# Kernel optimization log

Hardware: AMD Instinct MI355X
Metric: run time of the kernel (lower is better)

Reference implementation:

```python
import jax, jax.numpy as jnp
import numpy as np

B = 262144
L, NO, NW = 5, 5, 3          # num_layers, num_ops, num_widths
AD = L * NO * NW             # arch_dim = 75
D, H = 64, 4                 # embed_dim, num_heads
HD = D // H                  # head_dim = 16
EPS = 1e-5


def _ln(x, g, b):
    m = x.mean(-1, keepdims=True)
    v = ((x - m) ** 2).mean(-1, keepdims=True)
    return (x - m) / jnp.sqrt(v + EPS) * g + b


def setup_inputs() -> dict:
    key = jax.random.key(0)
    ks = jax.random.split(key, 16)
    s = 0.05
    return {
        "hw_idx": jax.random.randint(ks[0], (B,), 0, 4),
        "op_indices": jax.random.randint(ks[1], (B, L), 0, NO),
        "width_indices": jax.random.randint(ks[2], (B, L), 0, NW),
        "hw_embed": jax.random.normal(ks[3], (4, D)) * s,
        "W1": jax.random.normal(ks[4], (128, AD)) * s, "b1": jnp.zeros((128,)),
        "W2": jax.random.normal(ks[5], (D, 128)) * s, "b2": jnp.zeros((D,)),
        "ln1_g": jnp.ones((D,)), "ln1_b": jnp.zeros((D,)),
        "in_proj_w": jax.random.normal(ks[6], (3 * D, D)) * s,
        "in_proj_b": jnp.zeros((3 * D,)),
        "out_proj_w": jax.random.normal(ks[7], (D, D)) * s,
        "out_proj_b": jnp.zeros((D,)),
        "ln2_g": jnp.ones((D,)), "ln2_b": jnp.zeros((D,)),
        "W3": jax.random.normal(ks[8], (32, D)) * s, "b3": jnp.zeros((32,)),
        "W4": jax.random.normal(ks[9], (1, 32)) * s, "b4": jnp.zeros((1,)),
    }


def reference(hw_idx, op_indices, width_indices, hw_embed, W1, b1, W2, b2,
              ln1_g, ln1_b, in_proj_w, in_proj_b, out_proj_w, out_proj_b,
              ln2_g, ln2_b, W3, b3, W4, b4):
    # hardware embedding lookup -> [B, D]
    hw_emb = hw_embed[hw_idx]
    # vectorized one-hot arch encoding: [B, L*NO*NW]
    cell = op_indices * NW + width_indices                  # [B, L]
    onehot = jax.nn.one_hot(cell, NO * NW, dtype=jnp.float32).reshape(-1, AD)
    # arch encoder MLP + LayerNorm (dropout = identity at eval)
    h = jax.nn.relu(onehot @ W1.T + b1)
    arch_emb = _ln(h @ W2.T + b2, ln1_g, ln1_b)             # [B, D]
    # combined sequence of 2 tokens: [B, 2, D]
    combined = jnp.stack([hw_emb, arch_emb], axis=1)
    # multi-head self-attention (torch MultiheadAttention, batch_first)
    qkv = combined @ in_proj_w.T + in_proj_b                # [B, 2, 3D]
    q, k, v = jnp.split(qkv, 3, axis=-1)
    q = q.reshape(-1, 2, H, HD); k = k.reshape(-1, 2, H, HD); v = v.reshape(-1, 2, H, HD)
    scores = jnp.einsum('bqhd,bkhd->bhqk', q, k) / np.sqrt(HD)
    attn = jax.nn.softmax(scores, axis=-1)
    ctx = jnp.einsum('bhqk,bkhd->bqhd', attn, v).reshape(-1, 2, D)
    attn_out = ctx @ out_proj_w.T + out_proj_b
    # residual + LayerNorm, mean-pool over the 2 tokens
    x = _ln(attn_out + combined, ln2_g, ln2_b)
    pooled = x.mean(axis=1)                                 # [B, D]
    # prediction head
    latency = jax.nn.relu(pooled @ W3.T + b3) @ W4.T + b4   # [B, 1]
    return latency
```

## Files before the change

kernel.cpp:

```cpp
#include <hip/hip_runtime.h>


using s8v = __attribute__((ext_vector_type(8))) short;
using h8  = __attribute__((ext_vector_type(8))) _Float16;
using f4  = __attribute__((ext_vector_type(4))) float;

#define WF_W1   0
#define WF_W2   12288
#define WF_IP   20480
#define WF_OP   32768
#define WF_W3   36864
#define WF_HWE  38912

#define PWS     2304

__device__ __forceinline__ unsigned short f2h(float f) {
  _Float16 h = (_Float16)f;
  return __builtin_bit_cast(unsigned short, h);
}

__device__ __forceinline__ void swz(const float* __restrict__ W,
                                    const float* __restrict__ bias,
                                    unsigned short* __restrict__ dst,
                                    int Kreal, int KS, int NT, int t, int stride) {
  const int total = KS * NT * 512;
  for (int i = t; i < total; i += stride) {
    const int j = i & 7, ln = (i >> 3) & 63, fr = i >> 9;
    const int nt = fr % NT, ks = fr / NT;
    const int n = nt * 16 + (ln & 15);
    const int k = ks * 32 + (ln >> 4) * 8 + j;
    float v = 0.f;
    if (k < Kreal) v = W[n * Kreal + k];
    else if (bias && k == Kreal) v = bias[n];
    dst[i] = f2h(v);
  }
}

__global__ void k_pre(const float* __restrict__ hwe,
                      const float* __restrict__ W1, const float* __restrict__ b1,
                      const float* __restrict__ W2,
                      const float* __restrict__ ipw, const float* __restrict__ opw,
                      const float* __restrict__ W3,
                      unsigned short* __restrict__ ws) {
  const int t = blockIdx.x * 256 + threadIdx.x;
  const int stride = gridDim.x * 256;
  swz(W1,  b1,      ws + WF_W1, 75, 3, 8, t, stride);
  swz(W2,  nullptr, ws + WF_W2, 128, 4, 4, t, stride);
  swz(ipw, nullptr, ws + WF_IP, 64, 2, 12, t, stride);
  swz(opw, nullptr, ws + WF_OP, 64, 2, 4, t, stride);
  swz(W3,  nullptr, ws + WF_W3, 64, 2, 2, t, stride);
  for (int i = t; i < 256; i += stride) ws[WF_HWE + i] = f2h(hwe[i]);
}

__global__ __launch_bounds__(256, 4) void k_fused(
    const int* __restrict__ g_hw,
    const int* __restrict__ g_op, const int* __restrict__ g_wd,
    const float* __restrict__ g_hwe,
    const float* __restrict__ g_b2,
    const float* __restrict__ g_ln1g, const float* __restrict__ g_ln1b,
    const float* __restrict__ g_ipb, const float* __restrict__ g_opb,
    const float* __restrict__ g_ln2g, const float* __restrict__ g_ln2b,
    const float* __restrict__ g_b3,  const float* __restrict__ g_W4,
    const float* __restrict__ g_b4,
    const unsigned short* __restrict__ wsf,
    float* __restrict__ g_out) {
  __shared__ __align__(16) unsigned short sm[4 * PWS];
  const int tid = threadIdx.x;
  const int wave = tid >> 6, lane = tid & 63;
  const int quad = lane >> 4, l15 = lane & 15;
  unsigned short* pw = sm + wave * PWS;
  const int m0 = (blockIdx.x * 4 + wave) * 16;

  int hwv = 0, c0 = 0, c1 = 0, c2 = 0, c3 = 0, c4 = 0;
  if (lane < 16) {
    const int smp = m0 + lane;
    hwv = g_hw[smp];
    c0 =      g_op[smp * 5 + 0] * 3 + g_wd[smp * 5 + 0];
    c1 = 15 + g_op[smp * 5 + 1] * 3 + g_wd[smp * 5 + 1];
    c2 = 30 + g_op[smp * 5 + 2] * 3 + g_wd[smp * 5 + 2];
    c3 = 45 + g_op[smp * 5 + 3] * 3 + g_wd[smp * 5 + 3];
    c4 = 60 + g_op[smp * 5 + 4] * 3 + g_wd[smp * 5 + 4];
  }
  const int t0 = __shfl(c0, l15), t1 = __shfl(c1, l15), t2 = __shfl(c2, l15);
  const int t3 = __shfl(c3, l15), t4 = __shfl(c4, l15);
  const int hwrow = __shfl(hwv, l15);

  float b2v[4], l1gv[4], l1bv[4], opbv[4], l2gv[4], l2bv[4];
#pragma unroll
  for (int nt = 0; nt < 4; ++nt) {
    const int col = nt * 16 + l15;
    b2v[nt] = g_b2[col];  l1gv[nt] = g_ln1g[col]; l1bv[nt] = g_ln1b[col];
    opbv[nt] = g_opb[col]; l2gv[nt] = g_ln2g[col]; l2bv[nt] = g_ln2b[col];
  }
  float ipbq[4], ipbvv[4];
#pragma unroll
  for (int h = 0; h < 4; ++h) {
    ipbq[h]  = g_ipb[h * 16 + l15];
    ipbvv[h] = g_ipb[(h + 8) * 16 + l15];
  }
  float b3v[2], w4vv[2];
#pragma unroll
  for (int nt = 0; nt < 2; ++nt) {
    b3v[nt] = g_b3[nt * 16 + l15];
    w4vv[nt] = g_W4[nt * 16 + l15];
  }
  const float b4v = g_b4[0];

  h8 aoh[3];
#pragma unroll
  for (int ks = 0; ks < 3; ++ks) {
    s8v a;
#pragma unroll
    for (int j = 0; j < 8; ++j) {
      const int k = ks * 32 + quad * 8 + j;
      const bool hit = (k == 75) || (k == t0) || (k == t1) || (k == t2) ||
                       (k == t3) || (k == t4);
      a[j] = hit ? (short)0x3C00 : (short)0;
    }
    aoh[ks] = __builtin_bit_cast(h8, a);
  }

#pragma unroll
  for (int nt = 0; nt < 8; ++nt) {
    f4 acc = {0.f, 0.f, 0.f, 0.f};
#pragma unroll
    for (int ks = 0; ks < 3; ++ks) {
      const h8 bf = *(const h8*)(wsf + WF_W1 + ((ks * 8 + nt) * 64 + lane) * 8);
      acc = __builtin_amdgcn_mfma_f32_16x16x32_f16(aoh[ks], bf, acc, 0, 0, 0);
    }
    const int col = nt * 16 + l15;
#pragma unroll
    for (int r = 0; r < 4; ++r) {
      float v = acc[r];
      v = v > 0.f ? v : 0.f;
      pw[(quad * 4 + r) * 136 + col] = f2h(v);
    }
  }

  h8 a2[4];
#pragma unroll
  for (int ks = 0; ks < 4; ++ks)
    a2[ks] = *(const h8*)(pw + l15 * 136 + ks * 32 + quad * 8);
  float archres[4][4];
  {
    float val[4][4];
#pragma unroll
    for (int nt = 0; nt < 4; ++nt) {
      f4 acc = {0.f, 0.f, 0.f, 0.f};
#pragma unroll
      for (int ks = 0; ks < 4; ++ks) {
        const h8 bf = *(const h8*)(wsf + WF_W2 + ((ks * 4 + nt) * 64 + lane) * 8);
        acc = __builtin_amdgcn_mfma_f32_16x16x32_f16(a2[ks], bf, acc, 0, 0, 0);
      }
#pragma unroll
      for (int r = 0; r < 4; ++r) val[nt][r] = acc[r] + b2v[nt];
    }
#pragma unroll
    for (int r = 0; r < 4; ++r) {
      float s = val[0][r] + val[1][r] + val[2][r] + val[3][r];
      float q = val[0][r] * val[0][r] + val[1][r] * val[1][r] +
                val[2][r] * val[2][r] + val[3][r] * val[3][r];
#pragma unroll
      for (int off = 1; off <= 8; off <<= 1) {
        s += __shfl_xor(s, off);
        q += __shfl_xor(q, off);
      }
      const float mean = s * (1.f / 64.f);
      const float var  = q * (1.f / 64.f) - mean * mean;
      const float rstd = rsqrtf(var + 1e-5f);
#pragma unroll
      for (int nt = 0; nt < 4; ++nt) {
        const int col = nt * 16 + l15;
        const float xn = (val[nt][r] - mean) * rstd * l1gv[nt] + l1bv[nt];
        archres[nt][r] = xn;
        pw[(quad * 4 + r) * 72 + col] = f2h(xn);
      }
    }
  }

  h8 at0[2], at1[2];
#pragma unroll
  for (int ks = 0; ks < 2; ++ks) {
    at0[ks] = *(const h8*)(wsf + WF_HWE + hwrow * 64 + ks * 32 + quad * 8);
    at1[ks] = *(const h8*)(pw + l15 * 72 + ks * 32 + quad * 8);
  }
#pragma unroll
  for (int h = 0; h < 4; ++h) {
    f4 aq0 = {0.f,0.f,0.f,0.f}, aq1 = {0.f,0.f,0.f,0.f};
    f4 ak0 = {0.f,0.f,0.f,0.f}, ak1 = {0.f,0.f,0.f,0.f};
    f4 av0 = {0.f,0.f,0.f,0.f}, av1 = {0.f,0.f,0.f,0.f};
#pragma unroll
    for (int ks = 0; ks < 2; ++ks) {
      const h8 bq = *(const h8*)(wsf + WF_IP + ((ks * 12 + h    ) * 64 + lane) * 8);
      const h8 bk = *(const h8*)(wsf + WF_IP + ((ks * 12 + h + 4) * 64 + lane) * 8);
      const h8 bv = *(const h8*)(wsf + WF_IP + ((ks * 12 + h + 8) * 64 + lane) * 8);
      aq0 = __builtin_amdgcn_mfma_f32_16x16x32_f16(at0[ks], bq, aq0, 0, 0, 0);
      aq1 = __builtin_amdgcn_mfma_f32_16x16x32_f16(at1[ks], bq, aq1, 0, 0, 0);
      ak0 = __builtin_amdgcn_mfma_f32_16x16x32_f16(at0[ks], bk, ak0, 0, 0, 0);
      ak1 = __builtin_amdgcn_mfma_f32_16x16x32_f16(at1[ks], bk, ak1, 0, 0, 0);
      av0 = __builtin_amdgcn_mfma_f32_16x16x32_f16(at0[ks], bv, av0, 0, 0, 0);
      av1 = __builtin_amdgcn_mfma_f32_16x16x32_f16(at1[ks], bv, av1, 0, 0, 0);
    }
    float d0[4], d1[4], v0[4], v1[4];
#pragma unroll
    for (int r = 0; r < 4; ++r) {
      const float dk = ak1[r] - ak0[r];
      d0[r] = (aq0[r] + ipbq[h]) * dk;
      d1[r] = (aq1[r] + ipbq[h]) * dk;
      v0[r] = av0[r] + ipbvv[h];
      v1[r] = av1[r] + ipbvv[h];
    }
#pragma unroll
    for (int off = 1; off <= 8; off <<= 1)
#pragma unroll
      for (int r = 0; r < 4; ++r) {
        d0[r] += __shfl_xor(d0[r], off);
        d1[r] += __shfl_xor(d1[r], off);
      }
#pragma unroll
    for (int r = 0; r < 4; ++r) {
      const float a01 = 1.f / (1.f + __expf(-d0[r] * 0.25f));
      const float a11 = 1.f / (1.f + __expf(-d1[r] * 0.25f));
      const float dv = v1[r] - v0[r];
      const float ctx0 = v0[r] + a01 * dv;
      const float ctx1 = v0[r] + a11 * dv;
      const int col = h * 16 + l15;
      pw[(quad * 4 + r) * 72 + col]      = f2h(ctx0);
      pw[(16 + quad * 4 + r) * 72 + col] = f2h(ctx1);
    }
  }

  h8 ca[2][2];
#pragma unroll
  for (int mt = 0; mt < 2; ++mt)
#pragma unroll
    for (int ks = 0; ks < 2; ++ks)
      ca[mt][ks] = *(const h8*)(pw + (mt * 16 + l15) * 72 + ks * 32 + quad * 8);
  f4 oacc[2][4];
#pragma unroll
  for (int nt = 0; nt < 4; ++nt) {
    const h8 bf0 = *(const h8*)(wsf + WF_OP + ((0 * 4 + nt) * 64 + lane) * 8);
    const h8 bf1 = *(const h8*)(wsf + WF_OP + ((1 * 4 + nt) * 64 + lane) * 8);
#pragma unroll
    for (int mt = 0; mt < 2; ++mt) {
      f4 acc = {0.f, 0.f, 0.f, 0.f};
      acc = __builtin_amdgcn_mfma_f32_16x16x32_f16(ca[mt][0], bf0, acc, 0, 0, 0);
      acc = __builtin_amdgcn_mfma_f32_16x16x32_f16(ca[mt][1], bf1, acc, 0, 0, 0);
      oacc[mt][nt] = acc;
    }
  }
  float pool[4][4];
#pragma unroll
  for (int mt = 0; mt < 2; ++mt) {
    float val[4][4];
#pragma unroll
    for (int r = 0; r < 4; ++r) {
      if (mt == 0) {
        const int hr = __shfl(hwv, quad * 4 + r);
#pragma unroll
        for (int nt = 0; nt < 4; ++nt)
          val[nt][r] = oacc[0][nt][r] + opbv[nt] + g_hwe[hr * 64 + nt * 16 + l15];
      } else {
#pragma unroll
        for (int nt = 0; nt < 4; ++nt)
          val[nt][r] = oacc[1][nt][r] + opbv[nt] + archres[nt][r];
      }
    }
#pragma unroll
    for (int r = 0; r < 4; ++r) {
      float s = val[0][r] + val[1][r] + val[2][r] + val[3][r];
      float q = val[0][r] * val[0][r] + val[1][r] * val[1][r] +
                val[2][r] * val[2][r] + val[3][r] * val[3][r];
#pragma unroll
      for (int off = 1; off <= 8; off <<= 1) {
        s += __shfl_xor(s, off);
        q += __shfl_xor(q, off);
      }
      const float mean = s * (1.f / 64.f);
      const float var  = q * (1.f / 64.f) - mean * mean;
      const float rstd = rsqrtf(var + 1e-5f);
#pragma unroll
      for (int nt = 0; nt < 4; ++nt) {
        const float xn = (val[nt][r] - mean) * rstd * l2gv[nt] + l2bv[nt];
        if (mt == 0) pool[nt][r] = 0.5f * xn;
        else         pool[nt][r] += 0.5f * xn;
      }
    }
  }
#pragma unroll
  for (int nt = 0; nt < 4; ++nt)
#pragma unroll
    for (int r = 0; r < 4; ++r)
      pw[(quad * 4 + r) * 72 + nt * 16 + l15] = f2h(pool[nt][r]);

  h8 pa[2];
#pragma unroll
  for (int ks = 0; ks < 2; ++ks)
    pa[ks] = *(const h8*)(pw + l15 * 72 + ks * 32 + quad * 8);
  float part[4] = {0.f, 0.f, 0.f, 0.f};
#pragma unroll
  for (int nt = 0; nt < 2; ++nt) {
    const h8 bf0 = *(const h8*)(wsf + WF_W3 + ((0 * 2 + nt) * 64 + lane) * 8);
    const h8 bf1 = *(const h8*)(wsf + WF_W3 + ((1 * 2 + nt) * 64 + lane) * 8);
    f4 acc = {0.f, 0.f, 0.f, 0.f};
    acc = __builtin_amdgcn_mfma_f32_16x16x32_f16(pa[0], bf0, acc, 0, 0, 0);
    acc = __builtin_amdgcn_mfma_f32_16x16x32_f16(pa[1], bf1, acc, 0, 0, 0);
#pragma unroll
    for (int r = 0; r < 4; ++r) {
      float y = acc[r] + b3v[nt];
      y = y > 0.f ? y : 0.f;
      part[r] += y * w4vv[nt];
    }
  }
#pragma unroll
  for (int off = 1; off <= 8; off <<= 1)
#pragma unroll
    for (int r = 0; r < 4; ++r)
      part[r] += __shfl_xor(part[r], off);
  if (l15 == 0) {
#pragma unroll
    for (int r = 0; r < 4; ++r)
      g_out[m0 + quad * 4 + r] = part[r] + b4v;
  }
}

extern "C" void kernel_launch(void* const* d_in, const int* in_sizes, int n_in,
                              void* d_out, int out_size, void* d_ws, size_t ws_size,
                              hipStream_t stream) {
  (void)in_sizes; (void)n_in; (void)out_size; (void)ws_size;
  unsigned short* ws = (unsigned short*)d_ws;

  k_pre<<<64, 256, 0, stream>>>(
      (const float*)d_in[3], (const float*)d_in[4], (const float*)d_in[5],
      (const float*)d_in[6], (const float*)d_in[10], (const float*)d_in[12],
      (const float*)d_in[16], ws);

  k_fused<<<4096, 256, 0, stream>>>(
      (const int*)d_in[0],
      (const int*)d_in[1], (const int*)d_in[2],
      (const float*)d_in[3],
      (const float*)d_in[7],
      (const float*)d_in[8], (const float*)d_in[9],
      (const float*)d_in[11], (const float*)d_in[13],
      (const float*)d_in[14], (const float*)d_in[15],
      (const float*)d_in[17], (const float*)d_in[18],
      (const float*)d_in[19],
      ws, (float*)d_out);
}
```

Before: 172.4 us.

## Precompute hardware-token QKV tables and restructure attention with fdot2 per head

```diff
diff --git a/kernel.cpp b/kernel.cpp
--- a/kernel.cpp
+++ b/kernel.cpp
@@ -3,6 +3,7 @@
 
 using s8v = __attribute__((ext_vector_type(8))) short;
 using h8  = __attribute__((ext_vector_type(8))) _Float16;
+using h2v = __attribute__((ext_vector_type(2))) _Float16;
 using f4  = __attribute__((ext_vector_type(4))) float;
 
 #define WF_W1   0
@@ -11,12 +12,26 @@
 #define WF_OP   32768
 #define WF_W3   36864
 #define WF_HWE  38912
-
-#define PWS     2304
+#define TQ0     39168
+#define TK0     39424
+#define TV0B    39680
+#define TV0R    39936
+#define TBQ     40192
+
+#define PWS     3456
 
 __device__ __forceinline__ unsigned short f2h(float f) {
   _Float16 h = (_Float16)f;
   return __builtin_bit_cast(unsigned short, h);
+}
+
+__device__ __forceinline__ float dot8(h8 a, h8 b, float acc) {
+  const f4 af = __builtin_bit_cast(f4, a), bf = __builtin_bit_cast(f4, b);
+#pragma unroll
+  for (int u = 0; u < 4; ++u)
+    acc = __builtin_amdgcn_fdot2(__builtin_bit_cast(h2v, af[u]),
+                                 __builtin_bit_cast(h2v, bf[u]), acc, false);
+  return acc;
 }
 
 __device__ __forceinline__ void swz(const float* __restrict__ W,
@@ -39,7 +54,8 @@
 __global__ void k_pre(const float* __restrict__ hwe,
                       const float* __restrict__ W1, const float* __restrict__ b1,
                       const float* __restrict__ W2,
-                      const float* __restrict__ ipw, const float* __restrict__ opw,
+                      const float* __restrict__ ipw, const float* __restrict__ ipb,
+                      const float* __restrict__ opw,
                       const float* __restrict__ W3,
                       unsigned short* __restrict__ ws) {
   const int t = blockIdx.x * 256 + threadIdx.x;
@@ -50,6 +66,19 @@
   swz(opw, nullptr, ws + WF_OP, 64, 2, 4, t, stride);
   swz(W3,  nullptr, ws + WF_W3, 64, 2, 2, t, stride);
   for (int i = t; i < 256; i += stride) ws[WF_HWE + i] = f2h(hwe[i]);
+  for (int i = t; i < 768; i += stride) {
+    const int hw = i / 192, n = i - hw * 192;
+    const float* er = hwe + hw * 64;
+    const float* wr = ipw + (size_t)n * 64;
+    float acc = 0.f;
+#pragma unroll 8
+    for (int d = 0; d < 64; ++d) acc += er[d] * wr[d];
+    if (n < 64)       ws[TQ0  + hw * 64 + n]         = f2h(acc + ipb[n]);
+    else if (n < 128) ws[TK0  + hw * 64 + (n - 64)]  = f2h(acc);
+    else {            ws[TV0B + hw * 64 + (n - 128)] = f2h(acc + ipb[n]);
+                      ws[TV0R + hw * 64 + (n - 128)] = f2h(acc); }
+  }
+  for (int i = t; i < 64; i += stride) ws[TBQ + i] = f2h(ipb[i]);
 }
 
 __global__ __launch_bounds__(256, 4) void k_fused(
@@ -58,7 +87,7 @@
     const float* __restrict__ g_hwe,
     const float* __restrict__ g_b2,
     const float* __restrict__ g_ln1g, const float* __restrict__ g_ln1b,
-    const float* __restrict__ g_ipb, const float* __restrict__ g_opb,
+    const float* __restrict__ g_opb,
     const float* __restrict__ g_ln2g, const float* __restrict__ g_ln2b,
     const float* __restrict__ g_b3,  const float* __restrict__ g_W4,
     const float* __restrict__ g_b4,
@@ -92,12 +121,6 @@
     b2v[nt] = g_b2[col];  l1gv[nt] = g_ln1g[col]; l1bv[nt] = g_ln1b[col];
     opbv[nt] = g_opb[col]; l2gv[nt] = g_ln2g[col]; l2bv[nt] = g_ln2b[col];
   }
-  float ipbq[4], ipbvv[4];
-#pragma unroll
-  for (int h = 0; h < 4; ++h) {
-    ipbq[h]  = g_ipb[h * 16 + l15];
-    ipbvv[h] = g_ipb[(h + 8) * 16 + l15];
-  }
   float b3v[2], w4vv[2];
 #pragma unroll
   for (int nt = 0; nt < 2; ++nt) {
@@ -106,17 +129,26 @@
   }
   const float b4v = g_b4[0];
 
+  unsigned w0 = (1u << t0) | (1u << t1);
+  unsigned w1 = 1u << (t3 - 32);
+  unsigned w2 = 1u << 11;
+  {
+    const unsigned m2 = 1u << (t2 & 31);
+    w0 |= (t2 < 32) ? m2 : 0u;
+    w1 |= (t2 >= 32) ? m2 : 0u;
+    const unsigned m4 = 1u << (t4 & 31);
+    w1 |= (t4 < 64) ? m4 : 0u;
+    w2 |= (t4 >= 64) ? m4 : 0u;
+  }
   h8 aoh[3];
 #pragma unroll
   for (int ks = 0; ks < 3; ++ks) {
+    const unsigned wm = (ks == 0) ? w0 : (ks == 1) ? w1 : w2;
+    const unsigned sh = wm >> (quad * 8);
     s8v a;
 #pragma unroll
-    for (int j = 0; j < 8; ++j) {
-      const int k = ks * 32 + quad * 8 + j;
-      const bool hit = (k == 75) || (k == t0) || (k == t1) || (k == t2) ||
-                       (k == t3) || (k == t4);
-      a[j] = hit ? (short)0x3C00 : (short)0;
-    }
+    for (int j = 0; j < 8; ++j)
+      a[j] = ((sh >> j) & 1u) ? (short)0x3C00 : (short)0;
     aoh[ks] = __builtin_bit_cast(h8, a);
   }
 
@@ -178,56 +210,65 @@
     }
   }
 
-  h8 at0[2], at1[2];
-#pragma unroll
-  for (int ks = 0; ks < 2; ++ks) {
-    at0[ks] = *(const h8*)(wsf + WF_HWE + hwrow * 64 + ks * 32 + quad * 8);
+  h8 at1[2];
+#pragma unroll
+  for (int ks = 0; ks < 2; ++ks)
     at1[ks] = *(const h8*)(pw + l15 * 72 + ks * 32 + quad * 8);
-  }
 #pragma unroll
   for (int h = 0; h < 4; ++h) {
-    f4 aq0 = {0.f,0.f,0.f,0.f}, aq1 = {0.f,0.f,0.f,0.f};
-    f4 ak0 = {0.f,0.f,0.f,0.f}, ak1 = {0.f,0.f,0.f,0.f};
-    f4 av0 = {0.f,0.f,0.f,0.f}, av1 = {0.f,0.f,0.f,0.f};
+    f4 aq = {0.f,0.f,0.f,0.f}, ak = {0.f,0.f,0.f,0.f}, av = {0.f,0.f,0.f,0.f};
 #pragma unroll
     for (int ks = 0; ks < 2; ++ks) {
       const h8 bq = *(const h8*)(wsf + WF_IP + ((ks * 12 + h    ) * 64 + lane) * 8);
       const h8 bk = *(const h8*)(wsf + WF_IP + ((ks * 12 + h + 4) * 64 + lane) * 8);
       const h8 bv = *(const h8*)(wsf + WF_IP + ((ks * 12 + h + 8) * 64 + lane) * 8);
-      aq0 = __builtin_amdgcn_mfma_f32_16x16x32_f16(at0[ks], bq, aq0, 0, 0, 0);
-      aq1 = __builtin_amdgcn_mfma_f32_16x16x32_f16(at1[ks], bq, aq1, 0, 0, 0);
-      ak0 = __builtin_amdgcn_mfma_f32_16x16x32_f16(at0[ks], bk, ak0, 0, 0, 0);
-      ak1 = __builtin_amdgcn_mfma_f32_16x16x32_f16(at1[ks], bk, ak1, 0, 0, 0);
-      av0 = __builtin_amdgcn_mfma_f32_16x16x32_f16(at0[ks], bv, av0, 0, 0, 0);
-      av1 = __builtin_amdgcn_mfma_f32_16x16x32_f16(at1[ks], bv, av1, 0, 0, 0);
-    }
-    float d0[4], d1[4], v0[4], v1[4];
-#pragma unroll
-    for (int r = 0; r < 4; ++r) {
-      const float dk = ak1[r] - ak0[r];
-      d0[r] = (aq0[r] + ipbq[h]) * dk;
-      d1[r] = (aq1[r] + ipbq[h]) * dk;
-      v0[r] = av0[r] + ipbvv[h];
-      v1[r] = av1[r] + ipbvv[h];
-    }
-#pragma unroll
-    for (int off = 1; off <= 8; off <<= 1)
-#pragma unroll
-      for (int r = 0; r < 4; ++r) {
-        d0[r] += __shfl_xor(d0[r], off);
-        d1[r] += __shfl_xor(d1[r], off);
-      }
-#pragma unroll
-    for (int r = 0; r < 4; ++r) {
-      const float a01 = 1.f / (1.f + __expf(-d0[r] * 0.25f));
-      const float a11 = 1.f / (1.f + __expf(-d1[r] * 0.25f));
-      const float dv = v1[r] - v0[r];
-      const float ctx0 = v0[r] + a01 * dv;
-      const float ctx1 = v0[r] + a11 * dv;
-      const int col = h * 16 + l15;
-      pw[(quad * 4 + r) * 72 + col]      = f2h(ctx0);
-      pw[(16 + quad * 4 + r) * 72 + col] = f2h(ctx1);
-    }
+      aq = __builtin_amdgcn_mfma_f32_16x16x32_f16(at1[ks], bq, aq, 0, 0, 0);
+      ak = __builtin_amdgcn_mfma_f32_16x16x32_f16(at1[ks], bk, ak, 0, 0, 0);
+      av = __builtin_amdgcn_mfma_f32_16x16x32_f16(at1[ks], bv, av, 0, 0, 0);
+    }
+    const int col = h * 16 + l15;
+#pragma unroll
+    for (int r = 0; r < 4; ++r) {
+      const int row = quad * 4 + r;
+      pw[row * 72 + col]        = f2h(aq[r]);
+      pw[1152 + row * 72 + col] = f2h(ak[r]);
+      pw[2304 + row * 72 + col] = f2h(av[r]);
+    }
+  }
+
+  {
+    const int qb = quad * 16;
+    const unsigned short* q1p = pw + l15 * 72 + qb;
+    const h8 q1a = *(const h8*)(q1p),          q1b = *(const h8*)(q1p + 8);
+    const h8 k1a = *(const h8*)(q1p + 1152),   k1b = *(const h8*)(q1p + 1160);
+    const h8 v1a = *(const h8*)(q1p + 2304),   v1b = *(const h8*)(q1p + 2312);
+    const int tb = hwrow * 64 + qb;
+    const h8 Q0a = *(const h8*)(wsf + TQ0 + tb),  Q0b = *(const h8*)(wsf + TQ0 + tb + 8);
+    const h8 K0a = *(const h8*)(wsf + TK0 + tb),  K0b = *(const h8*)(wsf + TK0 + tb + 8);
+    const h8 VBa = *(const h8*)(wsf + TV0B + tb), VBb = *(const h8*)(wsf + TV0B + tb + 8);
+    const h8 VRa = *(const h8*)(wsf + TV0R + tb), VRb = *(const h8*)(wsf + TV0R + tb + 8);
+    const h8 bqa = *(const h8*)(wsf + TBQ + qb),  bqb = *(const h8*)(wsf + TBQ + qb + 8);
+    const h8 dka = k1a - K0a, dkb = k1b - K0b;
+    const float d0 = dot8(Q0a, dka, dot8(Q0b, dkb, 0.f));
+    const float d1 = dot8(q1a, dka, dot8(q1b, dkb,
+                     dot8(bqa, dka, dot8(bqb, dkb, 0.f))));
+    const float a01 = 1.f / (1.f + __expf(-d0 * 0.25f));
+    const float a11 = 1.f / (1.f + __expf(-d1 * 0.25f));
+    const h8 dva = v1a - VRa, dvb = v1b - VRb;
+    h8 c0a, c0b, c1a, c1b;
+#pragma unroll
+    for (int j = 0; j < 8; ++j) {
+      const float vb0 = (float)VBa[j], dv0 = (float)dva[j];
+      const float vb1 = (float)VBb[j], dv1 = (float)dvb[j];
+      c0a[j] = (_Float16)(vb0 + a01 * dv0);
+      c0b[j] = (_Float16)(vb1 + a01 * dv1);
+      c1a[j] = (_Float16)(vb0 + a11 * dv0);
+      c1b[j] = (_Float16)(vb1 + a11 * dv1);
+    }
+    *(h8*)(pw + l15 * 72 + qb)            = c0a;
+    *(h8*)(pw + l15 * 72 + qb + 8)        = c0b;
+    *(h8*)(pw + (16 + l15) * 72 + qb)     = c1a;
+    *(h8*)(pw + (16 + l15) * 72 + qb + 8) = c1b;
   }
 
   h8 ca[2][2];
@@ -332,8 +373,8 @@
 
   k_pre<<<64, 256, 0, stream>>>(
       (const float*)d_in[3], (const float*)d_in[4], (const float*)d_in[5],
-      (const float*)d_in[6], (const float*)d_in[10], (const float*)d_in[12],
-      (const float*)d_in[16], ws);
+      (const float*)d_in[6], (const float*)d_in[10], (const float*)d_in[11],
+      (const float*)d_in[12], (const float*)d_in[16], ws);
 
   k_fused<<<4096, 256, 0, stream>>>(
       (const int*)d_in[0],
@@ -341,7 +382,7 @@
       (const float*)d_in[3],
       (const float*)d_in[7],
       (const float*)d_in[8], (const float*)d_in[9],
-      (const float*)d_in[11], (const float*)d_in[13],
+      (const float*)d_in[13],
       (const float*)d_in[14], (const float*)d_in[15],
       (const float*)d_in[17], (const float*)d_in[18],
       (const float*)d_in[19],
```

Result: slower. 176.8 us (+2.6%).
